# Performance work log

Measured on AMD Instinct MI355X. Metric: run time of the kernel, lower is better.

## Reference

```python
import jax, jax.numpy as jnp
import numpy as np

B, C, N = 16, 256, 64  # batch, channels, input spatial (even, square)

def _blur_filter(channels, dtype):
    # filt_size=3 binomial: outer([1,2,1],[1,2,1]) normalized, tiled depthwise
    a = jnp.array([1.0, 2.0, 1.0], dtype=jnp.float32)
    f = a[:, None] * a[None, :]
    f = f / jnp.sum(f)
    return jnp.tile(f[None, None], (channels, 1, 1, 1)).astype(dtype)  # [C,1,3,3]

def setup_inputs() -> dict:
    key = jax.random.key(0)
    k1, k2 = jax.random.split(key)
    inp = jax.random.normal(k1, (B, C, N, N), dtype=jnp.float32)
    polyphase_indices = jax.random.randint(k2, (B,), 0, 4, dtype=jnp.int32)
    return {"inp": inp, "polyphase_indices": polyphase_indices}

def reference(inp, polyphase_indices):
    Bb, Cc, Nn, _ = inp.shape
    # Polyphase scatter: place inp into the selected one of 4 phases per batch.
    # Phase p = r + 2*c places x at y1[:, :, r::2, c::2] (p0=(0,0), p1=(1,0), p2=(0,1), p3=(1,1)).
    y = jnp.zeros((Bb, 4, Cc, Nn, Nn), inp.dtype)
    y = y.at[jnp.arange(Bb), polyphase_indices].set(inp)
    # Interleave phases into [B, C, 2N, 2N]
    yp = jnp.transpose(y, (0, 2, 3, 4, 1)).reshape(Bb, Cc, Nn, Nn, 2, 2)  # [..., i, j, c, r]
    y1 = jnp.transpose(yp, (0, 1, 2, 5, 3, 4)).reshape(Bb, Cc, 2 * Nn, 2 * Nn)
    # Circular pad by 1 on each spatial side (filt_size=3 -> pad_sizes [1,1,1,1])
    y1p = jnp.pad(y1, ((0, 0), (0, 0), (1, 1), (1, 1)), mode='wrap')
    # Depthwise blur conv, groups = C
    filt = _blur_filter(Cc, inp.dtype)
    out = jax.lax.conv_general_dilated(
        y1p, filt, window_strides=(1, 1), padding='VALID',
        dimension_numbers=('NCHW', 'OIHW', 'NCHW'), feature_group_count=Cc)
    return out  # [B, C, 2N, 2N]
```

## Files before the change

kernel.cpp:

```cpp
#include <hip/hip_runtime.h>


#define BB 16
#define CC 256
#define NN 64

__global__ __launch_bounds__(256) void aps_up_kernel(
    const float* __restrict__ inp,
    const int*   __restrict__ phase,
    float*       __restrict__ out)
{
    const int tid = blockIdx.x * 256 + threadIdx.x;

    const int lane_in_row = tid & 31;
    const int oy    = (tid >> 5) & 127;
    const int plane = tid >> 12;
    const int b     = plane >> 8;

    const int p = phase[b];
    const int r = p & 1;
    const int c = p >> 1;

    const int u  = (oy - r) & 127;
    const int i0 = u >> 1;
    const int i1 = ((u + 1) & 127) >> 1;

    const int ox0 = lane_in_row << 2;
    const int v0  = (ox0 - c) & 127;
    const int k0  = v0 >> 1;
    const int k1  = (k0 + 1) & 63;
    const int k2  = (k0 + 2) & 63;

    const float* base = inp + (size_t)plane * (NN * NN);
    const float* row0 = base + i0 * NN;
    const float* row1 = base + i1 * NN;

    const float s0 = row0[k0] + row1[k0];
    const float s1 = row0[k1] + row1[k1];
    const float s2 = row0[k2] + row1[k2];

    float4 o;
    if (c == 0) {
        o = make_float4(s0 + s0, s0 + s1, s1 + s1, s1 + s2);
    } else {
        o = make_float4(s0 + s1, s1 + s1, s1 + s2, s2 + s2);
    }
    const float sc = 0.0625f;
    o.x *= sc; o.y *= sc; o.z *= sc; o.w *= sc;

    reinterpret_cast<float4*>(out)[tid] = o;
}

extern "C" void kernel_launch(void* const* d_in, const int* in_sizes, int n_in,
                              void* d_out, int out_size, void* d_ws, size_t ws_size,
                              hipStream_t stream) {
    const float* inp   = (const float*)d_in[0];
    const int*   phase = (const int*)d_in[1];
    float*       out   = (float*)d_out;

    const int total_threads = out_size / 4;
    const int block = 256;
    const int grid  = total_threads / block;
    aps_up_kernel<<<grid, block, 0, stream>>>(inp, phase, out);
}
```

Before: 370.1 us.

## Vectorize input loads, produce eight outputs per thread with wave shuffles

Each thread now loads one float4 from each of two input rows and writes eight outputs as two float4 stores, instead of six scalar loads and one float4 store. The neighbouring column value needed at the edge is fetched from the adjacent lane with a wave shuffle, wrapping within the 16-lane row group. Output stores are marked nontemporal to avoid polluting cache, and the grid is halved. The kernel is memory bound, so the aim is fewer and wider memory instructions; the cost is shuffle overhead and reliance on 16 lanes mapping exactly to one input row.

```diff
diff --git a/kernel.cpp b/kernel.cpp
--- a/kernel.cpp
+++ b/kernel.cpp
@@ -1,20 +1,18 @@
 #include <hip/hip_runtime.h>
 
 
-#define BB 16
-#define CC 256
-#define NN 64
+typedef float v4f __attribute__((ext_vector_type(4)));
 
 __global__ __launch_bounds__(256) void aps_up_kernel(
     const float* __restrict__ inp,
     const int*   __restrict__ phase,
     float*       __restrict__ out)
 {
-    const int tid = blockIdx.x * 256 + threadIdx.x;
+    const int g = blockIdx.x * 256 + threadIdx.x;
 
-    const int lane_in_row = tid & 31;
-    const int oy    = (tid >> 5) & 127;
-    const int plane = tid >> 12;
+    const int j     = g & 15;
+    const int oy    = (g >> 4) & 127;
+    const int plane = g >> 11;
     const int b     = plane >> 8;
 
     const int p = phase[b];
@@ -25,30 +23,35 @@
     const int i0 = u >> 1;
     const int i1 = ((u + 1) & 127) >> 1;
 
-    const int ox0 = lane_in_row << 2;
-    const int v0  = (ox0 - c) & 127;
-    const int k0  = v0 >> 1;
-    const int k1  = (k0 + 1) & 63;
-    const int k2  = (k0 + 2) & 63;
+    const v4f* basef4 = reinterpret_cast<const v4f*>(inp) + (size_t)plane * 1024;
+    const v4f a = basef4[i0 * 16 + j];
+    const v4f d = basef4[i1 * 16 + j];
 
-    const float* base = inp + (size_t)plane * (NN * NN);
-    const float* row0 = base + i0 * NN;
-    const float* row1 = base + i1 * NN;
+    const v4f s = a + d;
+    const float s0 = s.x, s1 = s.y, s2 = s.z, s3 = s.w;
 
-    const float s0 = row0[k0] + row1[k0];
-    const float s1 = row0[k1] + row1[k1];
-    const float s2 = row0[k2] + row1[k2];
+    const int lane = threadIdx.x & 63;
+    const int grp  = lane & 48;
 
-    float4 o;
+    v4f o0, o1;
     if (c == 0) {
-        o = make_float4(s0 + s0, s0 + s1, s1 + s1, s1 + s2);
+        const int src = grp | ((j + 1) & 15);
+        const float s4 = __shfl(s0, src, 64);
+        o0 = (v4f){s0 + s0, s0 + s1, s1 + s1, s1 + s2};
+        o1 = (v4f){s2 + s2, s2 + s3, s3 + s3, s3 + s4};
     } else {
-        o = make_float4(s0 + s1, s1 + s1, s1 + s2, s2 + s2);
+        const int src = grp | ((j - 1) & 15);
+        const float sm1 = __shfl(s3, src, 64);
+        o0 = (v4f){sm1 + s0, s0 + s0, s0 + s1, s1 + s1};
+        o1 = (v4f){s1 + s2, s2 + s2, s2 + s3, s3 + s3};
     }
     const float sc = 0.0625f;
-    o.x *= sc; o.y *= sc; o.z *= sc; o.w *= sc;
+    o0 *= sc;
+    o1 *= sc;
 
-    reinterpret_cast<float4*>(out)[tid] = o;
+    v4f* outp = reinterpret_cast<v4f*>(out) + (size_t)g * 2;
+    __builtin_nontemporal_store(o0, outp);
+    __builtin_nontemporal_store(o1, outp + 1);
 }
 
 extern "C" void kernel_launch(void* const* d_in, const int* in_sizes, int n_in,
@@ -58,7 +61,7 @@
     const int*   phase = (const int*)d_in[1];
     float*       out   = (float*)d_out;
 
-    const int total_threads = out_size / 4;
+    const int total_threads = out_size / 8;
     const int block = 256;
     const int grid  = total_threads / block;
     aps_up_kernel<<<grid, block, 0, stream>>>(inp, phase, out);
```

Result: faster. 308.5 us (-16.7%).
